# Kernel optimization log

Measured on AMD Instinct MI355X. Metric: run time of the kernel, lower is better.

## Reference

```python
import jax, jax.numpy as jnp
import numpy as np

B, F, D = 16384, 40, 64  # batch, num_fields, embedding_size
D_OUT = 64               # att_embedding_size * head_num = 32 * 2


def setup_inputs() -> dict:
    key = jax.random.key(0)
    ks = jax.random.split(key, 5)
    return {
        "inputs": jax.random.normal(ks[0], (B, F, D), dtype=jnp.float32),
        "W_Query": jax.random.normal(ks[1], (D, D_OUT), dtype=jnp.float32) * 0.05,
        "W_key": jax.random.normal(ks[2], (D, D_OUT), dtype=jnp.float32) * 0.05,
        "W_Value": jax.random.normal(ks[3], (D, D_OUT), dtype=jnp.float32) * 0.05,
        "W_Res": jax.random.normal(ks[4], (D, D_OUT), dtype=jnp.float32) * 0.05,
    }


def reference(inputs, W_Query, W_key, W_Value, W_Res):
    # QKV projections (no head splitting, per original module)
    q = jnp.einsum('bfd,de->bfe', inputs, W_Query)  # [B, F, D_OUT]
    k = jnp.einsum('bfd,de->bfe', inputs, W_key)
    v = jnp.einsum('bfd,de->bfe', inputs, W_Value)
    # scaled-dot-product over the field axis; scaling=False so no divide
    scores = jax.nn.softmax(jnp.einsum('bqe,bke->bqk', q, k), axis=-1)  # [B, F, F]
    result = jnp.einsum('bqk,bke->bqe', scores, v)
    # residual projection (use_res=True)
    result = result + jnp.einsum('bfd,de->bfe', inputs, W_Res)
    return jax.nn.relu(result)
```

## Files before the change

### kernel.cpp

```cpp
#include <hip/hip_runtime.h>
#include <hip/hip_bf16.h>

#define BB  16384
#define F   40

typedef __bf16 bf16;
typedef __bf16 bf16x8 __attribute__((ext_vector_type(8)));
typedef __bf16 bf16x4 __attribute__((ext_vector_type(4)));
typedef short  s16x4  __attribute__((ext_vector_type(4)));
typedef float  f32x4  __attribute__((ext_vector_type(4)));


__device__ __forceinline__ bf16x8 cvt8(float4 a, float4 b) {
    bf16x8 f;
    f[0] = (bf16)a.x; f[1] = (bf16)a.y; f[2] = (bf16)a.z; f[3] = (bf16)a.w;
    f[4] = (bf16)b.x; f[5] = (bf16)b.y; f[6] = (bf16)b.z; f[7] = (bf16)b.w;
    return f;
}
__device__ __forceinline__ bf16x4 cvt4(float4 a) {
    bf16x4 f;
    f[0] = (bf16)a.x; f[1] = (bf16)a.y; f[2] = (bf16)a.z; f[3] = (bf16)a.w;
    return f;
}
__device__ __forceinline__ bf16x4 pack4(f32x4 a) {
    bf16x4 f;
    f[0] = (bf16)a[0]; f[1] = (bf16)a[1]; f[2] = (bf16)a[2]; f[3] = (bf16)a[3];
    return f;
}
__device__ __forceinline__ f32x4 mfma32(bf16x8 a, bf16x8 b, f32x4 c) {
    return __builtin_amdgcn_mfma_f32_16x16x32_bf16(a, b, c, 0, 0, 0);
}
__device__ __forceinline__ f32x4 mfma16(bf16x4 a, bf16x4 b, f32x4 c) {
#if __has_builtin(__builtin_amdgcn_mfma_f32_16x16x16_bf16)
    return __builtin_amdgcn_mfma_f32_16x16x16_bf16(a, b, c, 0, 0, 0);
#else
    return __builtin_amdgcn_mfma_f32_16x16x16bf16_1k(
        __builtin_bit_cast(s16x4, a), __builtin_bit_cast(s16x4, b), c, 0, 0, 0);
#endif
}

__global__ __launch_bounds__(256)
void prep_weights(const float* __restrict__ Wq, const float* __restrict__ Wk,
                  const float* __restrict__ Wv, const float* __restrict__ Wr,
                  bf16* __restrict__ ws)
{
    const int tid = threadIdx.x;
    if (blockIdx.x > 0) {
        const float* W = (blockIdx.x == 1) ? Wv : Wr;
        bf16* dst = ws + 4096 * blockIdx.x;
        for (int f = tid; f < 4096; f += 256) {
            int j = f & 7, ln = (f >> 3) & 63, kt = (f >> 9) & 1, nt = f >> 10;
            dst[f] = (bf16)W[(kt * 32 + (ln >> 4) * 8 + j) * 64 + nt * 16 + (ln & 15)];
        }
        return;
    }
    __shared__ float Gs[64 * 64];
    if (tid < 64) {
        const int l16 = tid & 15, quad = tid >> 4;
        bf16x8 aq[4][2], ak[4][2];
        #pragma unroll
        for (int mt = 0; mt < 4; ++mt)
            #pragma unroll
            for (int kt = 0; kt < 2; ++kt) {
                const float* pq = Wq + (mt * 16 + l16) * 64 + kt * 32 + quad * 8;
                const float* pk = Wk + (mt * 16 + l16) * 64 + kt * 32 + quad * 8;
                aq[mt][kt] = cvt8(*(const float4*)pq, *(const float4*)(pq + 4));
                ak[mt][kt] = cvt8(*(const float4*)pk, *(const float4*)(pk + 4));
            }
        #pragma unroll
        for (int mt = 0; mt < 4; ++mt)
            #pragma unroll
            for (int nt = 0; nt < 4; ++nt) {
                f32x4 acc = {0.f, 0.f, 0.f, 0.f};
                acc = mfma32(aq[mt][0], ak[nt][0], acc);
                acc = mfma32(aq[mt][1], ak[nt][1], acc);
                #pragma unroll
                for (int r = 0; r < 4; ++r)
                    Gs[(mt * 16 + quad * 4 + r) * 64 + nt * 16 + l16] = acc[r];
            }
    }
    __syncthreads();
    for (int f = tid; f < 4096; f += 256) {
        int j = f & 7, ln = (f >> 3) & 63, kt = (f >> 9) & 1, nt = f >> 10;
        ws[f] = (bf16)Gs[(kt * 32 + (ln >> 4) * 8 + j) * 64 + nt * 16 + (ln & 15)];
    }
}

__global__ __launch_bounds__(64, 4)
void attn_fused(const float* __restrict__ X, const bf16* __restrict__ wfrag,
                float* __restrict__ Out)
{
    const int lane = threadIdx.x;
    const int l16  = lane & 15;
    const int quad = lane >> 4;
    const float* Xb = X + (size_t)blockIdx.x * (F * 64);

    int rowm[3];
    #pragma unroll
    for (int mt = 0; mt < 3; ++mt) {
        int r = mt * 16 + l16; rowm[mt] = (r >= F) ? (F - 1) : r;
    }

    bf16x8 xf[3][2];
    #pragma unroll
    for (int mt = 0; mt < 3; ++mt)
        #pragma unroll
        for (int kt = 0; kt < 2; ++kt) {
            const float* p = Xb + rowm[mt] * 64 + kt * 32 + quad * 8;
            xf[mt][kt] = cvt8(*(const float4*)p, *(const float4*)(p + 4));
        }

    bf16x4 xa[3][4];
    #pragma unroll
    for (int mt = 0; mt < 3; ++mt)
        #pragma unroll
        for (int kt = 0; kt < 4; ++kt) {
            const float* p = Xb + rowm[mt] * 64 + kt * 16 + quad * 4;
            xa[mt][kt] = cvt4(*(const float4*)p);
        }

    const bf16x8* gF = (const bf16x8*)wfrag;
    const bf16x8* vF = gF + 512;
    const bf16x8* rF = gF + 1024;

    bf16x4 pkQ[4][3];
    #pragma unroll
    for (int mt = 0; mt < 4; ++mt) {
        bf16x8 a0 = gF[(mt * 2 + 0) * 64 + lane];
        bf16x8 a1 = gF[(mt * 2 + 1) * 64 + lane];
        #pragma unroll
        for (int nt = 0; nt < 3; ++nt) {
            f32x4 acc = {0.f, 0.f, 0.f, 0.f};
            acc = mfma32(a0, xf[nt][0], acc);
            acc = mfma32(a1, xf[nt][1], acc);
            pkQ[mt][nt] = pack4(acc);
        }
    }

    f32x4 sacc[3][3];
    #pragma unroll
    for (int mt = 0; mt < 3; ++mt)
        #pragma unroll
        for (int nt = 0; nt < 3; ++nt) {
            f32x4 acc = {0.f, 0.f, 0.f, 0.f};
            #pragma unroll
            for (int kt = 0; kt < 4; ++kt)
                acc = mfma16(xa[mt][kt], pkQ[kt][nt], acc);
            sacc[mt][nt] = acc;
        }

    const bool dead = (quad >= 2);
    bf16x4 pkP[3][3];
    #pragma unroll
    for (int nt = 0; nt < 3; ++nt) {
        float ex[3][4]; float sum = 0.f;
        #pragma unroll
        for (int mt = 0; mt < 3; ++mt)
            #pragma unroll
            for (int r = 0; r < 4; ++r) {
                float e = (mt == 2 && dead) ? 0.f : __expf(sacc[mt][nt][r]);
                ex[mt][r] = e; sum += e;
            }
        sum += __shfl_xor(sum, 16, 64);
        sum += __shfl_xor(sum, 32, 64);
        float inv = 1.0f / sum;
        #pragma unroll
        for (int mt = 0; mt < 3; ++mt) {
            bf16x4 pk;
            pk[0] = (bf16)(ex[mt][0] * inv); pk[1] = (bf16)(ex[mt][1] * inv);
            pk[2] = (bf16)(ex[mt][2] * inv); pk[3] = (bf16)(ex[mt][3] * inv);
            pkP[mt][nt] = pk;
        }
    }

    bf16x4 pkV[3][4];
    #pragma unroll
    for (int nt = 0; nt < 4; ++nt) {
        bf16x8 b0 = vF[(nt * 2 + 0) * 64 + lane];
        bf16x8 b1 = vF[(nt * 2 + 1) * 64 + lane];
        #pragma unroll
        for (int mt = 0; mt < 3; ++mt) {
            f32x4 acc = {0.f, 0.f, 0.f, 0.f};
            acc = mfma32(xf[mt][0], b0, acc);
            acc = mfma32(xf[mt][1], b1, acc);
            pkV[mt][nt] = pack4(acc);
        }
    }

    float* Ob = Out + (size_t)blockIdx.x * (F * 64);
    #pragma unroll
    for (int half = 0; half < 2; ++half) {
        f32x4 oacc[2][3];
        #pragma unroll
        for (int me = 0; me < 2; ++me) {
            int mt = half * 2 + me;
            bf16x8 a0 = rF[(mt * 2 + 0) * 64 + lane];
            bf16x8 a1 = rF[(mt * 2 + 1) * 64 + lane];
            #pragma unroll
            for (int nt = 0; nt < 3; ++nt) {
                f32x4 acc = {0.f, 0.f, 0.f, 0.f};
                acc = mfma32(a0, xf[nt][0], acc);
                acc = mfma32(a1, xf[nt][1], acc);
                oacc[me][nt] = acc;
            }
        }
        #pragma unroll
        for (int me = 0; me < 2; ++me) {
            int mt = half * 2 + me;
            #pragma unroll
            for (int nt = 0; nt < 3; ++nt) {
                f32x4 acc = oacc[me][nt];
                #pragma unroll
                for (int kt = 0; kt < 3; ++kt)
                    acc = mfma16(pkV[kt][mt], pkP[kt][nt], acc);
                oacc[me][nt] = acc;
            }
        }
        #pragma unroll
        for (int nt = 0; nt < 3; ++nt) {
            int m = nt * 16 + l16;
            if (m < F) {
                #pragma unroll
                for (int me = 0; me < 2; ++me) {
                    f32x4 st;
                    st[0] = fmaxf(oacc[me][nt][0], 0.f); st[1] = fmaxf(oacc[me][nt][1], 0.f);
                    st[2] = fmaxf(oacc[me][nt][2], 0.f); st[3] = fmaxf(oacc[me][nt][3], 0.f);
                    __builtin_nontemporal_store(st,
                        (f32x4*)&Ob[m * 64 + (half * 2 + me) * 16 + quad * 4]);
                }
            }
        }
    }
}

extern "C" void kernel_launch(void* const* d_in, const int* in_sizes, int n_in,
                              void* d_out, int out_size, void* d_ws, size_t ws_size,
                              hipStream_t stream) {
    const float* X  = (const float*)d_in[0];
    const float* Wq = (const float*)d_in[1];
    const float* Wk = (const float*)d_in[2];
    const float* Wv = (const float*)d_in[3];
    const float* Wr = (const float*)d_in[4];
    float* Out = (float*)d_out;
    bf16* ws = (bf16*)d_ws;

    prep_weights<<<3, 256, 0, stream>>>(Wq, Wk, Wv, Wr, ws);
    attn_fused<<<BB, 64, 0, stream>>>(X, ws, Out);
}
```

Before: 333.8 us.

## Stage weights in LDS and software-pipeline X loads over persistent per-wave batches

The single-wave-per-block kernel becomes 8-wave blocks in which each wave handles 4 consecutive batch items. Weight fragments are copied once per block into shared memory instead of being re-read from global memory for every item. X is coalesced-loaded, converted to bf16 and staged in a padded per-wave LDS buffer, and the next item's X loads are interleaved with the current item's MFMA work. This cuts redundant weight traffic and hides load latency, at the cost of more LDS use and register pressure, which may lower occupancy.

```diff
diff --git a/kernel.cpp b/kernel.cpp
--- a/kernel.cpp
+++ b/kernel.cpp
@@ -1,8 +1,11 @@
 #include <hip/hip_runtime.h>
 #include <hip/hip_bf16.h>
 
-#define BB  16384
-#define F   40
+#define BB   16384
+#define F    40
+#define WPB  8
+#define NBW  4
+#define XROW 72
 
 typedef __bf16 bf16;
 typedef __bf16 bf16x8 __attribute__((ext_vector_type(8)));
@@ -11,15 +14,15 @@
 typedef float  f32x4  __attribute__((ext_vector_type(4)));
 
 
+__device__ __forceinline__ bf16x4 cvt4(float4 a) {
+    bf16x4 f;
+    f[0] = (bf16)a.x; f[1] = (bf16)a.y; f[2] = (bf16)a.z; f[3] = (bf16)a.w;
+    return f;
+}
 __device__ __forceinline__ bf16x8 cvt8(float4 a, float4 b) {
     bf16x8 f;
     f[0] = (bf16)a.x; f[1] = (bf16)a.y; f[2] = (bf16)a.z; f[3] = (bf16)a.w;
     f[4] = (bf16)b.x; f[5] = (bf16)b.y; f[6] = (bf16)b.z; f[7] = (bf16)b.w;
-    return f;
-}
-__device__ __forceinline__ bf16x4 cvt4(float4 a) {
-    bf16x4 f;
-    f[0] = (bf16)a.x; f[1] = (bf16)a.y; f[2] = (bf16)a.z; f[3] = (bf16)a.w;
     return f;
 }
 __device__ __forceinline__ bf16x4 pack4(f32x4 a) {
@@ -86,14 +89,34 @@
     }
 }
 
-__global__ __launch_bounds__(64, 4)
+__global__ __launch_bounds__(64 * WPB)
 void attn_fused(const float* __restrict__ X, const bf16* __restrict__ wfrag,
                 float* __restrict__ Out)
 {
-    const int lane = threadIdx.x;
+    __shared__ bf16 WS[3 * 4096];
+    __shared__ bf16 XS[WPB][F * XROW];
+
+    const int tid  = threadIdx.x;
+    const int lane = tid & 63;
+    const int wav  = tid >> 6;
     const int l16  = lane & 15;
     const int quad = lane >> 4;
-    const float* Xb = X + (size_t)blockIdx.x * (F * 64);
+
+    {
+        const float4* src = (const float4*)wfrag;
+        float4* dst = (float4*)WS;
+        #pragma unroll
+        for (int j = 0; j < 3; ++j)
+            dst[tid + 512 * j] = src[tid + 512 * j];
+    }
+    __syncthreads();
+
+    bf16* XSw  = &XS[wav][0];
+    bf16* sdst = XSw + quad * XROW + l16 * 4;
+
+    const bf16* gL = WS           + lane * 8;
+    const bf16* vL = WS + 4096    + lane * 8;
+    const bf16* rL = WS + 2*4096  + lane * 8;
 
     int rowm[3];
     #pragma unroll
@@ -101,132 +124,156 @@
         int r = mt * 16 + l16; rowm[mt] = (r >= F) ? (F - 1) : r;
     }
 
-    bf16x8 xf[3][2];
-    #pragma unroll
-    for (int mt = 0; mt < 3; ++mt)
-        #pragma unroll
-        for (int kt = 0; kt < 2; ++kt) {
-            const float* p = Xb + rowm[mt] * 64 + kt * 32 + quad * 8;
-            xf[mt][kt] = cvt8(*(const float4*)p, *(const float4*)(p + 4));
-        }
-
-    bf16x4 xa[3][4];
-    #pragma unroll
-    for (int mt = 0; mt < 3; ++mt)
-        #pragma unroll
-        for (int kt = 0; kt < 4; ++kt) {
-            const float* p = Xb + rowm[mt] * 64 + kt * 16 + quad * 4;
-            xa[mt][kt] = cvt4(*(const float4*)p);
-        }
-
-    const bf16x8* gF = (const bf16x8*)wfrag;
-    const bf16x8* vF = gF + 512;
-    const bf16x8* rF = gF + 1024;
-
-    bf16x4 pkQ[4][3];
-    #pragma unroll
-    for (int mt = 0; mt < 4; ++mt) {
-        bf16x8 a0 = gF[(mt * 2 + 0) * 64 + lane];
-        bf16x8 a1 = gF[(mt * 2 + 1) * 64 + lane];
-        #pragma unroll
-        for (int nt = 0; nt < 3; ++nt) {
-            f32x4 acc = {0.f, 0.f, 0.f, 0.f};
-            acc = mfma32(a0, xf[nt][0], acc);
-            acc = mfma32(a1, xf[nt][1], acc);
-            pkQ[mt][nt] = pack4(acc);
-        }
-    }
-
-    f32x4 sacc[3][3];
-    #pragma unroll
-    for (int mt = 0; mt < 3; ++mt)
-        #pragma unroll
-        for (int nt = 0; nt < 3; ++nt) {
-            f32x4 acc = {0.f, 0.f, 0.f, 0.f};
+    const size_t b0 = ((size_t)blockIdx.x * WPB + wav) * NBW;
+
+    {
+        const float* Xs = X + b0 * (F * 64) + lane * 4;
+        float4 xr[10];
+        #pragma unroll
+        for (int t = 0; t < 10; ++t) xr[t] = *(const float4*)(Xs + t * 256);
+        #pragma unroll
+        for (int t = 0; t < 10; ++t) *(bf16x4*)(sdst + t * 4 * XROW) = cvt4(xr[t]);
+    }
+
+    #pragma unroll 1
+    for (int i = 0; i < NBW; ++i) {
+        const size_t b = b0 + i;
+        const bool more = (i + 1 < NBW);
+        const float* Xn = X + (b + 1) * (F * 64) + lane * 4;
+
+        bf16x8 xf[3][2];
+        bf16x4 xa[3][4];
+        #pragma unroll
+        for (int mt = 0; mt < 3; ++mt) {
+            const bf16* rb = XSw + rowm[mt] * XROW;
+            #pragma unroll
+            for (int kt = 0; kt < 2; ++kt)
+                xf[mt][kt] = *(const bf16x8*)(rb + kt * 32 + quad * 8);
             #pragma unroll
             for (int kt = 0; kt < 4; ++kt)
-                acc = mfma16(xa[mt][kt], pkQ[kt][nt], acc);
-            sacc[mt][nt] = acc;
-        }
-
-    const bool dead = (quad >= 2);
-    bf16x4 pkP[3][3];
-    #pragma unroll
-    for (int nt = 0; nt < 3; ++nt) {
-        float ex[3][4]; float sum = 0.f;
-        #pragma unroll
-        for (int mt = 0; mt < 3; ++mt)
-            #pragma unroll
-            for (int r = 0; r < 4; ++r) {
-                float e = (mt == 2 && dead) ? 0.f : __expf(sacc[mt][nt][r]);
-                ex[mt][r] = e; sum += e;
-            }
-        sum += __shfl_xor(sum, 16, 64);
-        sum += __shfl_xor(sum, 32, 64);
-        float inv = 1.0f / sum;
-        #pragma unroll
-        for (int mt = 0; mt < 3; ++mt) {
-            bf16x4 pk;
-            pk[0] = (bf16)(ex[mt][0] * inv); pk[1] = (bf16)(ex[mt][1] * inv);
-            pk[2] = (bf16)(ex[mt][2] * inv); pk[3] = (bf16)(ex[mt][3] * inv);
-            pkP[mt][nt] = pk;
-        }
-    }
-
-    bf16x4 pkV[3][4];
-    #pragma unroll
-    for (int nt = 0; nt < 4; ++nt) {
-        bf16x8 b0 = vF[(nt * 2 + 0) * 64 + lane];
-        bf16x8 b1 = vF[(nt * 2 + 1) * 64 + lane];
-        #pragma unroll
-        for (int mt = 0; mt < 3; ++mt) {
-            f32x4 acc = {0.f, 0.f, 0.f, 0.f};
-            acc = mfma32(xf[mt][0], b0, acc);
-            acc = mfma32(xf[mt][1], b1, acc);
-            pkV[mt][nt] = pack4(acc);
-        }
-    }
-
-    float* Ob = Out + (size_t)blockIdx.x * (F * 64);
-    #pragma unroll
-    for (int half = 0; half < 2; ++half) {
-        f32x4 oacc[2][3];
-        #pragma unroll
-        for (int me = 0; me < 2; ++me) {
-            int mt = half * 2 + me;
-            bf16x8 a0 = rF[(mt * 2 + 0) * 64 + lane];
-            bf16x8 a1 = rF[(mt * 2 + 1) * 64 + lane];
+                xa[mt][kt] = *(const bf16x4*)(rb + kt * 16 + quad * 4);
+        }
+
+        bf16x4 pkQ[4][3];
+        #pragma unroll
+        for (int mt = 0; mt < 4; ++mt) {
+            bf16x8 a0 = *(const bf16x8*)(gL + (mt * 2 + 0) * 512);
+            bf16x8 a1 = *(const bf16x8*)(gL + (mt * 2 + 1) * 512);
             #pragma unroll
             for (int nt = 0; nt < 3; ++nt) {
                 f32x4 acc = {0.f, 0.f, 0.f, 0.f};
                 acc = mfma32(a0, xf[nt][0], acc);
                 acc = mfma32(a1, xf[nt][1], acc);
-                oacc[me][nt] = acc;
-            }
-        }
-        #pragma unroll
-        for (int me = 0; me < 2; ++me) {
-            int mt = half * 2 + me;
-            #pragma unroll
-            for (int nt = 0; nt < 3; ++nt) {
-                f32x4 acc = oacc[me][nt];
+                pkQ[mt][nt] = pack4(acc);
+            }
+        }
+
+        f32x4 sacc[3][3];
+        #pragma unroll
+        for (int mt = 0; mt < 3; ++mt)
+            #pragma unroll
+            for (int nt = 0; nt < 3; ++nt) {
+                f32x4 acc = {0.f, 0.f, 0.f, 0.f};
+                #pragma unroll
+                for (int kt = 0; kt < 4; ++kt)
+                    acc = mfma16(xa[mt][kt], pkQ[kt][nt], acc);
+                sacc[mt][nt] = acc;
+            }
+
+        const bool dead = (quad >= 2);
+        bf16x4 pkP[3][3];
+        #pragma unroll
+        for (int nt = 0; nt < 3; ++nt) {
+            float ex[3][4]; float sum = 0.f;
+            #pragma unroll
+            for (int mt = 0; mt < 3; ++mt)
+                #pragma unroll
+                for (int r = 0; r < 4; ++r) {
+                    float e = (mt == 2 && dead) ? 0.f : __expf(sacc[mt][nt][r]);
+                    ex[mt][r] = e; sum += e;
+                }
+            sum += __shfl_xor(sum, 16, 64);
+            sum += __shfl_xor(sum, 32, 64);
+            float inv = 1.0f / sum;
+            #pragma unroll
+            for (int mt = 0; mt < 3; ++mt) {
+                bf16x4 pk;
+                pk[0] = (bf16)(ex[mt][0] * inv); pk[1] = (bf16)(ex[mt][1] * inv);
+                pk[2] = (bf16)(ex[mt][2] * inv); pk[3] = (bf16)(ex[mt][3] * inv);
+                pkP[mt][nt] = pk;
+            }
+        }
+
+        float4 xrA[5];
+        if (more) {
+            #pragma unroll
+            for (int t = 0; t < 5; ++t) xrA[t] = *(const float4*)(Xn + t * 256);
+        }
+
+        bf16x4 pkV[3][4];
+        #pragma unroll
+        for (int nt = 0; nt < 4; ++nt) {
+            bf16x8 b0w = *(const bf16x8*)(vL + (nt * 2 + 0) * 512);
+            bf16x8 b1w = *(const bf16x8*)(vL + (nt * 2 + 1) * 512);
+            #pragma unroll
+            for (int mt = 0; mt < 3; ++mt) {
+                f32x4 acc = {0.f, 0.f, 0.f, 0.f};
+                acc = mfma32(xf[mt][0], b0w, acc);
+                acc = mfma32(xf[mt][1], b1w, acc);
+                pkV[mt][nt] = pack4(acc);
+            }
+        }
+
+        float4 xrB[5];
+        if (more) {
+            #pragma unroll
+            for (int t = 0; t < 5; ++t) *(bf16x4*)(sdst + t * 4 * XROW) = cvt4(xrA[t]);
+            #pragma unroll
+            for (int t = 0; t < 5; ++t) xrB[t] = *(const float4*)(Xn + (5 + t) * 256);
+        }
+
+        f32x4 oacc[4][3];
+        #pragma unroll
+        for (int mt = 0; mt < 4; ++mt) {
+            bf16x8 a0 = *(const bf16x8*)(rL + (mt * 2 + 0) * 512);
+            bf16x8 a1 = *(const bf16x8*)(rL + (mt * 2 + 1) * 512);
+            #pragma unroll
+            for (int nt = 0; nt < 3; ++nt) {
+                f32x4 acc = {0.f, 0.f, 0.f, 0.f};
+                acc = mfma32(a0, xf[nt][0], acc);
+                acc = mfma32(a1, xf[nt][1], acc);
+                oacc[mt][nt] = acc;
+            }
+        }
+
+        if (more) {
+            #pragma unroll
+            for (int t = 0; t < 5; ++t) *(bf16x4*)(sdst + (5 + t) * 4 * XROW) = cvt4(xrB[t]);
+        }
+
+        #pragma unroll
+        for (int mt = 0; mt < 4; ++mt)
+            #pragma unroll
+            for (int nt = 0; nt < 3; ++nt) {
+                f32x4 acc = oacc[mt][nt];
                 #pragma unroll
                 for (int kt = 0; kt < 3; ++kt)
                     acc = mfma16(pkV[kt][mt], pkP[kt][nt], acc);
-                oacc[me][nt] = acc;
-            }
-        }
+                oacc[mt][nt] = acc;
+            }
+
+        float* Ob = Out + b * (F * 64);
         #pragma unroll
         for (int nt = 0; nt < 3; ++nt) {
             int m = nt * 16 + l16;
             if (m < F) {
                 #pragma unroll
-                for (int me = 0; me < 2; ++me) {
+                for (int mt = 0; mt < 4; ++mt) {
                     f32x4 st;
-                    st[0] = fmaxf(oacc[me][nt][0], 0.f); st[1] = fmaxf(oacc[me][nt][1], 0.f);
-                    st[2] = fmaxf(oacc[me][nt][2], 0.f); st[3] = fmaxf(oacc[me][nt][3], 0.f);
+                    st[0] = fmaxf(oacc[mt][nt][0], 0.f); st[1] = fmaxf(oacc[mt][nt][1], 0.f);
+                    st[2] = fmaxf(oacc[mt][nt][2], 0.f); st[3] = fmaxf(oacc[mt][nt][3], 0.f);
                     __builtin_nontemporal_store(st,
-                        (f32x4*)&Ob[m * 64 + (half * 2 + me) * 16 + quad * 4]);
+                        (f32x4*)&Ob[m * 64 + mt * 16 + quad * 4]);
                 }
             }
         }
@@ -245,5 +292,5 @@
     bf16* ws = (bf16*)d_ws;
 
     prep_weights<<<3, 256, 0, stream>>>(Wq, Wk, Wv, Wr, ws);
-    attn_fused<<<BB, 64, 0, stream>>>(X, ws, Out);
-}
+    attn_fused<<<BB / (WPB * NBW), 64 * WPB, 0, stream>>>(X, ws, Out);
+}
```

Result: slower. 401.7 us (+20.3%).
